# Kernel optimization log

Measured on AMD Instinct MI355X. Metric: run time of the kernel, lower is better.

## Reference

```python
import jax, jax.numpy as jnp
import numpy as np

B, S, H, NH = 2, 2048, 1024, 16
HD = H // NH  # head size = 64


def setup_inputs() -> dict:
    key = jax.random.key(0)
    ks = jax.random.split(key, 6)
    x = jax.random.normal(ks[0], (B, S, H), dtype=jnp.float32)
    additive_attention_mask = jnp.zeros((S,), dtype=jnp.float32)
    # nn.Linear params: weight [out, in], bias [out]
    w_qkv = jax.random.normal(ks[1], (3 * H, H), dtype=jnp.float32) / np.sqrt(H)
    b_qkv = jax.random.normal(ks[2], (3 * H,), dtype=jnp.float32) * 0.02
    w_o = jax.random.normal(ks[3], (H, H), dtype=jnp.float32) / np.sqrt(H)
    b_o = jax.random.normal(ks[4], (H,), dtype=jnp.float32) * 0.02
    return {"x": x, "additive_attention_mask": additive_attention_mask,
            "w_qkv": w_qkv, "b_qkv": b_qkv, "w_o": w_o, "b_o": b_o}


def reference(x, additive_attention_mask, w_qkv, b_qkv, w_o, b_o):
    # QKV projection: (B,S,H) @ (H,3H) + (3H,)
    qkv = jnp.einsum('bsh,oh->bso', x, w_qkv) + b_qkv
    q, k, v = qkv[..., :H], qkv[..., H:2 * H], qkv[..., 2 * H:]
    # split heads -> (B, NH, S, HD)
    def heads(t):
        return t.reshape(B, S, NH, HD).transpose(0, 2, 1, 3)
    qh, kh, vh = heads(q), heads(k), heads(v)
    # scores (B, NH, Sq, Sk); mask added BEFORE the 1/sqrt(d) scaling (faithful)
    scores = jnp.einsum('bhqd,bhkd->bhqk', qh, kh)
    scores = scores + additive_attention_mask[None, None, None, :]
    probs = jax.nn.softmax(scores / np.sqrt(HD).astype(np.float32), axis=-1)
    # dropout p=0.0 -> identity
    av = jnp.einsum('bhqk,bhkd->bqhd', probs, vh).reshape(B, S, H)
    return jnp.einsum('bsh,oh->bso', av, w_o) + b_o
```

## Files before the change

### kernel.cpp

```cpp
#include <hip/hip_runtime.h>
#include <cmath>

#define B_  2
#define S_  2048
#define H_  1024
#define NH_ 16
#define HD_ 64

typedef _Float16 half8  __attribute__((ext_vector_type(8)));
typedef __fp16   fp16x2 __attribute__((ext_vector_type(2)));
typedef float    f32x16 __attribute__((ext_vector_type(16)));

#define MFMA32(a, b, c) __builtin_amdgcn_mfma_f32_32x32x16_f16((a), (b), (c), 0, 0, 0)

__device__ __forceinline__ void gl2lds16(const void* g, void* l) {
    __builtin_amdgcn_global_load_lds(
        (const __attribute__((address_space(1))) unsigned int*)g,
        (__attribute__((address_space(3))) unsigned int*)l,
        16, 0, 0);
}

__device__ __forceinline__ unsigned pk16(float a, float b) {
    union { fp16x2 v; unsigned u; } c;
    c.v = __builtin_amdgcn_cvt_pkrtz(a, b);
    return c.u;
}

__device__ __forceinline__ float exp2_hw(float x) {
#if __has_builtin(__builtin_amdgcn_exp2f)
    return __builtin_amdgcn_exp2f(x);
#else
    return __expf(x * 0.6931471805599453f);
#endif
}

#define LOG2E   1.4426950408889634f
#define SCALE_  (0.125f * LOG2E)
#define THR2_   11.5415603f

__global__ __launch_bounds__(256, 4)
void conv_hilo(const float* __restrict__ src, _Float16* __restrict__ dh,
               _Float16* __restrict__ dl, int K)
{
    const int bid = blockIdx.x;
    const int nkt = K >> 6;
    const int rt  = bid / nkt;
    const int kt  = bid % nkt;
    const int tid = threadIdx.x;
    const size_t tb = (size_t)bid * 8192;
#pragma unroll
    for (int p = 0; p < 4; ++p) {
        const int idx = p * 256 + tid;
        const int r   = idx >> 3;
        const int g   = idx & 7;
        const float* s = src + (size_t)(rt * 128 + r) * K + kt * 64 + g * 8;
        const float4 v0 = *reinterpret_cast<const float4*>(s);
        const float4 v1 = *reinterpret_cast<const float4*>(s + 4);
        const float f[8] = {v0.x, v0.y, v0.z, v0.w, v1.x, v1.y, v1.z, v1.w};
        half8 hi, lo;
#pragma unroll
        for (int e = 0; e < 8; ++e) {
            const _Float16 hv = (_Float16)f[e];
            hi[e] = hv;
            lo[e] = (_Float16)(f[e] - (float)hv);
        }
        const int dst = r * 64 + ((g ^ (r & 7)) << 3);
        *reinterpret_cast<half8*>(dh + tb + dst) = hi;
        *reinterpret_cast<half8*>(dl + tb + dst) = lo;
    }
}

template<int QKV>
__global__ __launch_bounds__(256, 1)
void hgemm_split(const _Float16* __restrict__ Ah, const _Float16* __restrict__ Al,
                 const _Float16* __restrict__ Wh, const _Float16* __restrict__ Wl,
                 const float* __restrict__ bias, float* __restrict__ C,
                 float* __restrict__ Qo,
                 _Float16* __restrict__ Kh, _Float16* __restrict__ Kl,
                 _Float16* __restrict__ Vh, _Float16* __restrict__ Vl,
                 int nbm, int nbn, int nkt, int N)
{
    __shared__ __align__(16) unsigned char smem[131072];

    const int tid  = threadIdx.x;
    const int w    = tid >> 6;
    const int lane = tid & 63;
    const int lr   = lane & 31;
    const int hh   = lane >> 5;
    const int wm   = w >> 1, wn = w & 1;

    const int nwg = nbm * nbn;
    const int cpx = nwg >> 3;
    const int bid = blockIdx.x;
    const int wg  = (bid & 7) * cpx + (bid >> 3);
    const int mt  = wg / nbn, nt = wg % nbn;

    const size_t aBase = (size_t)mt * nkt * 8192;
    const size_t wBase = (size_t)nt * nkt * 8192;

    f32x16 acc[2][2];
#pragma unroll
    for (int mi = 0; mi < 2; ++mi)
#pragma unroll
        for (int ni = 0; ni < 2; ++ni)
#pragma unroll
            for (int r = 0; r < 16; ++r) acc[mi][ni][r] = 0.f;

    auto stage = [&](int kt, int buf) {
        const size_t at = aBase + (size_t)kt * 8192;
        const size_t wt = wBase + (size_t)kt * 8192;
        unsigned char* sb = smem + (buf << 16);
#pragma unroll
        for (int c = 0; c < 4; ++c) {
            const int loff = (w * 4 + c) * 512;
            const int goff = loff + lane * 8;
            gl2lds16((const void*)(Ah + at + goff), (void*)((_Float16*)sb + loff));
            gl2lds16((const void*)(Al + at + goff), (void*)((_Float16*)(sb + 16384) + loff));
            gl2lds16((const void*)(Wh + wt + goff), (void*)((_Float16*)(sb + 32768) + loff));
            gl2lds16((const void*)(Wl + wt + goff), (void*)((_Float16*)(sb + 49152) + loff));
        }
    };

    stage(0, 0);
    __syncthreads();

    for (int kt = 0; kt < nkt; ++kt) {
        if (kt + 1 < nkt) stage(kt + 1, (kt + 1) & 1);

        unsigned char* sb = smem + ((kt & 1) << 16);
        _Float16* sAh = (_Float16*)(sb);
        _Float16* sAl = (_Float16*)(sb + 16384);
        _Float16* sWh = (_Float16*)(sb + 32768);
        _Float16* sWl = (_Float16*)(sb + 49152);

#pragma unroll
        for (int ks = 0; ks < 4; ++ks) {
            const int g = ks * 2 + hh;
            half8 aH[2], aL[2], bH[2], bL[2];
#pragma unroll
            for (int mi = 0; mi < 2; ++mi) {
                const int r   = wm * 64 + mi * 32 + lr;
                const int idx = r * 64 + ((g ^ (r & 7)) << 3);
                aH[mi] = *reinterpret_cast<const half8*>(sAh + idx);
                aL[mi] = *reinterpret_cast<const half8*>(sAl + idx);
            }
#pragma unroll
            for (int ni = 0; ni < 2; ++ni) {
                const int c   = wn * 64 + ni * 32 + lr;
                const int idx = c * 64 + ((g ^ (c & 7)) << 3);
                bH[ni] = *reinterpret_cast<const half8*>(sWh + idx);
                bL[ni] = *reinterpret_cast<const half8*>(sWl + idx);
            }
#pragma unroll
            for (int mi = 0; mi < 2; ++mi)
#pragma unroll
                for (int ni = 0; ni < 2; ++ni) {
                    acc[mi][ni] = MFMA32(aH[mi], bH[ni], acc[mi][ni]);
                    acc[mi][ni] = MFMA32(aH[mi], bL[ni], acc[mi][ni]);
                    acc[mi][ni] = MFMA32(aL[mi], bH[ni], acc[mi][ni]);
                }
        }
        __syncthreads();
    }

    if constexpr (QKV == 0) {
        const int n0 = nt * 128 + wn * 64 + lr;
        float bv[2];
#pragma unroll
        for (int ni = 0; ni < 2; ++ni) bv[ni] = bias[n0 + ni * 32];
#pragma unroll
        for (int mi = 0; mi < 2; ++mi)
#pragma unroll
            for (int ni = 0; ni < 2; ++ni)
#pragma unroll
                for (int r = 0; r < 16; ++r) {
                    const int m = mt * 128 + wm * 64 + mi * 32 +
                                  (r & 3) + 8 * (r >> 2) + 4 * hh;
                    C[(size_t)m * N + n0 + ni * 32] = acc[mi][ni][r] + bv[ni];
                }
    } else {
        float* sC = (float*)smem;
        const int m0  = mt * 128;
        const int b   = m0 >> 11;
        const int kt0 = (m0 & 2047) >> 6;
#pragma unroll
        for (int pass = 0; pass < 2; ++pass) {
            __syncthreads();
            if (wm == pass) {
#pragma unroll
                for (int mi = 0; mi < 2; ++mi)
#pragma unroll
                    for (int ni = 0; ni < 2; ++ni)
#pragma unroll
                        for (int r = 0; r < 16; ++r) {
                            const int ml = mi * 32 + (r & 3) + 8 * (r >> 2) + 4 * hh;
                            sC[ml * 132 + wn * 64 + ni * 32 + lr] = acc[mi][ni][r];
                        }
            }
            __syncthreads();
            const int ktile = kt0 + pass;
            if (nt < 8) {
#pragma unroll
                for (int it = 0; it < 8; ++it) {
                    const int idx = it * 256 + tid;
                    const int row = idx >> 5;
                    const int c4  = (idx & 31) << 2;
                    float4 v = *reinterpret_cast<const float4*>(&sC[row * 132 + c4]);
                    const float4 bv = *reinterpret_cast<const float4*>(bias + nt * 128 + c4);
                    v.x += bv.x; v.y += bv.y; v.z += bv.z; v.w += bv.w;
                    *reinterpret_cast<float4*>(
                        Qo + (size_t)(m0 + pass * 64 + row) * 1024 + nt * 128 + c4) = v;
                }
            } else if (nt < 16) {
#pragma unroll
                for (int it = 0; it < 4; ++it) {
                    const int idx = it * 256 + tid;
                    const int key = idx >> 4;
                    const int g   = idx & 15;
                    const int head = 2 * (nt - 8) + (g >> 3);
                    const int d0   = (g & 7) << 3;
                    float f[8];
#pragma unroll
                    for (int e = 0; e < 8; ++e)
                        f[e] = sC[key * 132 + g * 8 + e] +
                               bias[1024 + (nt - 8) * 128 + g * 8 + e];
                    half8 hi, lo;
#pragma unroll
                    for (int e = 0; e < 8; ++e) {
                        const _Float16 hv = (_Float16)f[e];
                        hi[e] = hv;
                        lo[e] = (_Float16)(f[e] - (float)hv);
                    }
                    const size_t base = ((size_t)(b * 16 + head) * 32 + ktile) * 4096;
                    const size_t dst  = base + key * 64 + (d0 ^ ((key & 7) << 3));
                    *reinterpret_cast<half8*>(Kh + dst) = hi;
                    *reinterpret_cast<half8*>(Kl + dst) = lo;
                }
            } else {
#pragma unroll
                for (int it = 0; it < 4; ++it) {
                    const int idx = it * 256 + tid;
                    const int f   = idx >> 3;
                    const int kg  = idx & 7;
                    const int head = 2 * (nt - 16) + (f >> 6);
                    const int d    = f & 63;
                    const float bv = bias[2048 + (nt - 16) * 128 + f];
                    float fe[8];
#pragma unroll
                    for (int e = 0; e < 8; ++e)
                        fe[e] = sC[(kg * 8 + e) * 132 + f] + bv;
                    half8 hi, lo;
#pragma unroll
                    for (int e = 0; e < 8; ++e) {
                        const _Float16 hv = (_Float16)fe[e];
                        hi[e] = hv;
                        lo[e] = (_Float16)(fe[e] - (float)hv);
                    }
                    const size_t base = ((size_t)(b * 16 + head) * 32 + ktile) * 4096;
                    const size_t dst  = base + d * 64 + ((kg * 8) ^ ((d & 7) << 3));
                    *reinterpret_cast<half8*>(Vh + dst) = hi;
                    *reinterpret_cast<half8*>(Vl + dst) = lo;
                }
            }
        }
    }
}

__global__ __launch_bounds__(256, 2)
void attn_mfma(const float* __restrict__ Q, const float* __restrict__ mask,
               const _Float16* __restrict__ Kh, const _Float16* __restrict__ Kl,
               const _Float16* __restrict__ Vh, const _Float16* __restrict__ Vl,
               _Float16* __restrict__ Avh, _Float16* __restrict__ Avl)
{
    __shared__ __align__(16) unsigned char smem[73728];
    float* sM = (float*)(smem + 65536);
    float* sO = (float*)(smem);

    const int tid  = threadIdx.x;
    const int w    = tid >> 6;
    const int lane = tid & 63;
    const int lq   = lane & 31;
    const int hh   = lane >> 5;

    const int bid = blockIdx.x;
    const int wg  = (bid & 7) * 64 + (bid >> 3);
    const int bh  = wg >> 4;
    const int qb  = wg & 15;
    const int b   = bh >> 4, h = bh & 15;

    {
        const float4* mg = reinterpret_cast<const float4*>(mask);
        float4* ms = reinterpret_cast<float4*>(sM);
        float4 a = mg[tid], c = mg[tid + 256];
        a.x *= SCALE_; a.y *= SCALE_; a.z *= SCALE_; a.w *= SCALE_;
        c.x *= SCALE_; c.y *= SCALE_; c.z *= SCALE_; c.w *= SCALE_;
        ms[tid] = a; ms[tid + 256] = c;
    }

    const int qrow = b * S_ + qb * 128 + w * 32 + lq;
    half8 qh[4], ql[4];
#pragma unroll
    for (int ks = 0; ks < 4; ++ks) {
        const float* qp = Q + (size_t)qrow * 1024 + h * HD_ + ks * 16 + hh * 8;
        const float4 a = *reinterpret_cast<const float4*>(qp);
        const float4 c = *reinterpret_cast<const float4*>(qp + 4);
        float qf[8] = {a.x, a.y, a.z, a.w, c.x, c.y, c.z, c.w};
#pragma unroll
        for (int e = 0; e < 8; ++e) {
            const float sv = qf[e] * SCALE_;
            const _Float16 hv = (_Float16)sv;
            qh[ks][e] = hv;
            ql[ks][e] = (_Float16)(sv - (float)hv);
        }
    }

    const int swz = (lq & 7) << 3;
    int off[2][4];
#pragma unroll
    for (int t2 = 0; t2 < 2; ++t2)
#pragma unroll
        for (int ks = 0; ks < 4; ++ks)
            off[t2][ks] = (t2 * 32 + lq) * 64 + ((ks * 16 + hh * 8) ^ swz);

    f32x16 o0 = {0,0,0,0,0,0,0,0,0,0,0,0,0,0,0,0};
    f32x16 o1 = {0,0,0,0,0,0,0,0,0,0,0,0,0,0,0,0};
    float m_run = -INFINITY, l_run = 0.f;

    const size_t bhbase = (size_t)bh * 32 * 4096;

    {
        const size_t tb = bhbase;
#pragma unroll
        for (int i = 0; i < 2; ++i) {
            const int loff = (w * 2 + i) * 512;
            const int goff = loff + lane * 8;
            _Float16* nb = (_Float16*)smem;
            gl2lds16((const void*)(Kh + tb + goff), (void*)(nb + loff));
            gl2lds16((const void*)(Kl + tb + goff), (void*)(nb + 4096 + loff));
            gl2lds16((const void*)(Vh + tb + goff), (void*)(nb + 8192 + loff));
            gl2lds16((const void*)(Vl + tb + goff), (void*)(nb + 12288 + loff));
        }
    }
    __syncthreads();

    for (int kt = 0; kt < 32; ++kt) {
        _Float16* bb = (_Float16*)(smem + ((kt & 1) << 15));
        if (kt < 31) {
            _Float16* nb = (_Float16*)(smem + (((kt + 1) & 1) << 15));
            const size_t tb = bhbase + (size_t)(kt + 1) * 4096;
#pragma unroll
            for (int i = 0; i < 2; ++i) {
                const int loff = (w * 2 + i) * 512;
                const int goff = loff + lane * 8;
                gl2lds16((const void*)(Kh + tb + goff), (void*)(nb + loff));
                gl2lds16((const void*)(Kl + tb + goff), (void*)(nb + 4096 + loff));
                gl2lds16((const void*)(Vh + tb + goff), (void*)(nb + 8192 + loff));
                gl2lds16((const void*)(Vl + tb + goff), (void*)(nb + 12288 + loff));
            }
        }

        f32x16 st[2];
#pragma unroll
        for (int ktt = 0; ktt < 2; ++ktt) {
            f32x16 acc = {0,0,0,0,0,0,0,0,0,0,0,0,0,0,0,0};
#pragma unroll
            for (int ks = 0; ks < 4; ++ks) {
                const half8 ka = *reinterpret_cast<const half8*>(bb + off[ktt][ks]);
                const half8 kb = *reinterpret_cast<const half8*>(bb + 4096 + off[ktt][ks]);
                acc = MFMA32(ka, qh[ks], acc);
                acc = MFMA32(ka, ql[ks], acc);
                acc = MFMA32(kb, qh[ks], acc);
            }
            st[ktt] = acc;
        }

        float mx = -INFINITY;
#pragma unroll
        for (int ktt = 0; ktt < 2; ++ktt) {
#pragma unroll
            for (int rr = 0; rr < 4; ++rr) {
                const int key0 = kt * 64 + ktt * 32 + rr * 8 + hh * 4;
                const float4 mk = *reinterpret_cast<const float4*>(sM + key0);
                const float mkv[4] = {mk.x, mk.y, mk.z, mk.w};
#pragma unroll
                for (int c = 0; c < 4; ++c) {
                    const int r = rr * 4 + c;
                    const float tv = st[ktt][r] + mkv[c];
                    st[ktt][r] = tv;
                    mx = fmaxf(mx, tv);
                }
            }
        }
        mx = fmaxf(mx, __shfl_xor(mx, 32));

        if (!__all(mx - m_run <= THR2_)) {
            const float mnew = fmaxf(m_run, mx);
            const float corr = exp2_hw(m_run - mnew);
            m_run = mnew;
            l_run *= corr;
#pragma unroll
            for (int r = 0; r < 16; ++r) { o0[r] *= corr; o1[r] *= corr; }
        }
        float ps = 0.f;
#pragma unroll
        for (int ktt = 0; ktt < 2; ++ktt)
#pragma unroll
            for (int r = 0; r < 16; ++r) {
                const float p = exp2_hw(st[ktt][r] - m_run);
                st[ktt][r] = p;
                ps += p;
            }
        ps += __shfl_xor(ps, 32);
        l_run += ps;

        unsigned wph[2][4][2], wpl[2][4][2];
#pragma unroll
        for (int ktt = 0; ktt < 2; ++ktt)
#pragma unroll
            for (int rr = 0; rr < 4; ++rr)
#pragma unroll
                for (int pp = 0; pp < 2; ++pp) {
                    const float p0 = st[ktt][rr * 4 + pp * 2 + 0];
                    const float p1 = st[ktt][rr * 4 + pp * 2 + 1];
                    union { fp16x2 v; unsigned u; } hw;
                    hw.v = __builtin_amdgcn_cvt_pkrtz(p0, p1);
                    wph[ktt][rr][pp] = hw.u;
                    wpl[ktt][rr][pp] = pk16(p0 - (float)hw.v[0], p1 - (float)hw.v[1]);
                }

#pragma unroll
        for (int ks = 0; ks < 4; ++ks) {
            const int i1 = ks >> 1;
            const int rA = (ks & 1) * 2;
            union { unsigned u[4]; half8 v; } ph, pl;
            {
                const unsigned oA0 = wph[i1][rA + 0][0], oB0 = wph[i1][rA + 0][1];
                const unsigned oA1 = wph[i1][rA + 1][0], oB1 = wph[i1][rA + 1][1];
                const unsigned sA1 = (unsigned)__shfl_xor((int)oA1, 32);
                const unsigned sB1 = (unsigned)__shfl_xor((int)oB1, 32);
                const unsigned sA0 = (unsigned)__shfl_xor((int)oA0, 32);
                const unsigned sB0 = (unsigned)__shfl_xor((int)oB0, 32);
                ph.u[0] = hh ? sA1 : oA0;
                ph.u[1] = hh ? sB1 : oB0;
                ph.u[2] = hh ? oA1 : sA0;
                ph.u[3] = hh ? oB1 : sB0;
            }
            {
                const unsigned oA0 = wpl[i1][rA + 0][0], oB0 = wpl[i1][rA + 0][1];
                const unsigned oA1 = wpl[i1][rA + 1][0], oB1 = wpl[i1][rA + 1][1];
                const unsigned sA1 = (unsigned)__shfl_xor((int)oA1, 32);
                const unsigned sB1 = (unsigned)__shfl_xor((int)oB1, 32);
                const unsigned sA0 = (unsigned)__shfl_xor((int)oA0, 32);
                const unsigned sB0 = (unsigned)__shfl_xor((int)oB0, 32);
                pl.u[0] = hh ? sA1 : oA0;
                pl.u[1] = hh ? sB1 : oB0;
                pl.u[2] = hh ? oA1 : sA0;
                pl.u[3] = hh ? oB1 : sB0;
            }
#pragma unroll
            for (int dt = 0; dt < 2; ++dt) {
                const half8 va = *reinterpret_cast<const half8*>(bb + 8192 + off[dt][ks]);
                const half8 vb = *reinterpret_cast<const half8*>(bb + 12288 + off[dt][ks]);
                if (dt == 0) {
                    o0 = MFMA32(va, ph.v, o0);
                    o0 = MFMA32(va, pl.v, o0);
                    o0 = MFMA32(vb, ph.v, o0);
                } else {
                    o1 = MFMA32(va, ph.v, o1);
                    o1 = MFMA32(va, pl.v, o1);
                    o1 = MFMA32(vb, ph.v, o1);
                }
            }
        }
        __syncthreads();
    }

    const float inv = 1.f / l_run;
#pragma unroll
    for (int dt = 0; dt < 2; ++dt)
#pragma unroll
        for (int r = 0; r < 16; ++r) {
            const int d = dt * 32 + (r & 3) + 8 * (r >> 2) + 4 * hh;
            sO[(w * 32 + lq) * 68 + d] = (dt ? o1[r] : o0[r]) * inv;
        }
    __syncthreads();
    {
        const size_t tb = (((size_t)(b * 16 + qb)) * 16 + h) * 8192;
#pragma unroll
        for (int p = 0; p < 4; ++p) {
            const int idx = p * 256 + tid;
            const int q = idx >> 3, g = idx & 7;
            const float4 v0 = *reinterpret_cast<const float4*>(&sO[q * 68 + g * 8]);
            const float4 v1 = *reinterpret_cast<const float4*>(&sO[q * 68 + g * 8 + 4]);
            const float f[8] = {v0.x, v0.y, v0.z, v0.w, v1.x, v1.y, v1.z, v1.w};
            half8 hi, lo;
#pragma unroll
            for (int e = 0; e < 8; ++e) {
                const _Float16 hv = (_Float16)f[e];
                hi[e] = hv;
                lo[e] = (_Float16)(f[e] - (float)hv);
            }
            const int dst = q * 64 + ((g ^ (q & 7)) << 3);
            *reinterpret_cast<half8*>(Avh + tb + dst) = hi;
            *reinterpret_cast<half8*>(Avl + tb + dst) = lo;
        }
    }
}

extern "C" void kernel_launch(void* const* d_in, const int* in_sizes, int n_in,
                              void* d_out, int out_size, void* d_ws, size_t ws_size,
                              hipStream_t stream)
{
    const float* x     = (const float*)d_in[0];
    const float* mask  = (const float*)d_in[1];
    const float* w_qkv = (const float*)d_in[2];
    const float* b_qkv = (const float*)d_in[3];
    const float* w_o   = (const float*)d_in[4];
    const float* b_o   = (const float*)d_in[5];
    float* out = (float*)d_out;

    char* p = (char*)d_ws;
    float*    Qarr = (float*)p;             p += (size_t)4096 * 1024 * 4;
    _Float16* Kh   = (_Float16*)p;          p += (size_t)32 * 32 * 4096 * 2;
    _Float16* Kl   = (_Float16*)p;          p += (size_t)32 * 32 * 4096 * 2;
    _Float16* Vh   = (_Float16*)p;          p += (size_t)32 * 32 * 4096 * 2;
    _Float16* Vl   = (_Float16*)p;          p += (size_t)32 * 32 * 4096 * 2;
    _Float16* Xh   = (_Float16*)p;          p += (size_t)4096 * 1024 * 2;
    _Float16* Xl   = (_Float16*)p;          p += (size_t)4096 * 1024 * 2;
    _Float16* Wqh  = (_Float16*)p;          p += (size_t)3072 * 1024 * 2;
    _Float16* Wql  = (_Float16*)p;          p += (size_t)3072 * 1024 * 2;
    _Float16* Woh  = (_Float16*)p;          p += (size_t)1024 * 1024 * 2;
    _Float16* Wol  = (_Float16*)p;          p += (size_t)1024 * 1024 * 2;
    _Float16* Avh  = (_Float16*)p;          p += (size_t)4096 * 1024 * 2;
    _Float16* Avl  = (_Float16*)p;          p += (size_t)4096 * 1024 * 2;

    const dim3 blk(256);
    conv_hilo<<<dim3(32 * 16), blk, 0, stream>>>(x,     Xh,  Xl,  1024);
    conv_hilo<<<dim3(24 * 16), blk, 0, stream>>>(w_qkv, Wqh, Wql, 1024);
    conv_hilo<<<dim3(8 * 16),  blk, 0, stream>>>(w_o,   Woh, Wol, 1024);

    hgemm_split<1><<<dim3(32 * 24), blk, 0, stream>>>(
        Xh, Xl, Wqh, Wql, b_qkv, nullptr, Qarr, Kh, Kl, Vh, Vl, 32, 24, 16, 3072);
    attn_mfma<<<dim3(512), blk, 0, stream>>>(Qarr, mask, Kh, Kl, Vh, Vl, Avh, Avl);
    hgemm_split<0><<<dim3(32 * 8), blk, 0, stream>>>(
        Avh, Avl, Woh, Wol, b_o, out, nullptr, nullptr, nullptr, nullptr, nullptr,
        32, 8, 16, 1024);
}
```

Measured before the change: 335.3 us.

## Use 8 waves per GEMM block and drop low-half P term in attention

The split-fp16 GEMM moves from 4 to 8 waves per 128x128 tile. Each wave now owns a 32x64 sub-tile with two accumulators instead of four, and the staging and epilogue loops are retuned for 512 threads. The goal is more latency hiding and lower register pressure per wave. Separately, the attention P·V product no longer splits P into hi/lo fp16 parts, which drops one MFMA per pair and the matching shuffles. That trades some accuracy of the probabilities for fewer matrix operations.

```diff
diff --git a/kernel.cpp b/kernel.cpp
--- a/kernel.cpp
+++ b/kernel.cpp
@@ -71,7 +71,7 @@
 }
 
 template<int QKV>
-__global__ __launch_bounds__(256, 1)
+__global__ __launch_bounds__(512, 1)
 void hgemm_split(const _Float16* __restrict__ Ah, const _Float16* __restrict__ Al,
                  const _Float16* __restrict__ Wh, const _Float16* __restrict__ Wl,
                  const float* __restrict__ bias, float* __restrict__ C,
@@ -87,7 +87,8 @@
     const int lane = tid & 63;
     const int lr   = lane & 31;
     const int hh   = lane >> 5;
-    const int wm   = w >> 1, wn = w & 1;
+    const int wm   = w >> 1;
+    const int wn   = w & 1;
 
     const int nwg = nbm * nbn;
     const int cpx = nwg >> 3;
@@ -98,26 +99,23 @@
     const size_t aBase = (size_t)mt * nkt * 8192;
     const size_t wBase = (size_t)nt * nkt * 8192;
 
-    f32x16 acc[2][2];
-#pragma unroll
-    for (int mi = 0; mi < 2; ++mi)
-#pragma unroll
-        for (int ni = 0; ni < 2; ++ni)
-#pragma unroll
-            for (int r = 0; r < 16; ++r) acc[mi][ni][r] = 0.f;
+    f32x16 acc[2];
+#pragma unroll
+    for (int ni = 0; ni < 2; ++ni)
+#pragma unroll
+        for (int r = 0; r < 16; ++r) acc[ni][r] = 0.f;
 
     auto stage = [&](int kt, int buf) {
         const size_t at = aBase + (size_t)kt * 8192;
         const size_t wt = wBase + (size_t)kt * 8192;
         unsigned char* sb = smem + (buf << 16);
 #pragma unroll
-        for (int c = 0; c < 4; ++c) {
-            const int loff = (w * 4 + c) * 512;
-            const int goff = loff + lane * 8;
-            gl2lds16((const void*)(Ah + at + goff), (void*)((_Float16*)sb + loff));
-            gl2lds16((const void*)(Al + at + goff), (void*)((_Float16*)(sb + 16384) + loff));
-            gl2lds16((const void*)(Wh + wt + goff), (void*)((_Float16*)(sb + 32768) + loff));
-            gl2lds16((const void*)(Wl + wt + goff), (void*)((_Float16*)(sb + 49152) + loff));
+        for (int c = 0; c < 2; ++c) {
+            const int off = (c * 512 + tid) * 8;
+            gl2lds16((const void*)(Ah + at + off), (void*)((_Float16*)sb + off));
+            gl2lds16((const void*)(Al + at + off), (void*)((_Float16*)(sb + 16384) + off));
+            gl2lds16((const void*)(Wh + wt + off), (void*)((_Float16*)(sb + 32768) + off));
+            gl2lds16((const void*)(Wl + wt + off), (void*)((_Float16*)(sb + 49152) + off));
         }
     };
 
@@ -136,14 +134,11 @@
 #pragma unroll
         for (int ks = 0; ks < 4; ++ks) {
             const int g = ks * 2 + hh;
-            half8 aH[2], aL[2], bH[2], bL[2];
-#pragma unroll
-            for (int mi = 0; mi < 2; ++mi) {
-                const int r   = wm * 64 + mi * 32 + lr;
-                const int idx = r * 64 + ((g ^ (r & 7)) << 3);
-                aH[mi] = *reinterpret_cast<const half8*>(sAh + idx);
-                aL[mi] = *reinterpret_cast<const half8*>(sAl + idx);
-            }
+            const int r = wm * 32 + lr;
+            const int aidx = r * 64 + ((g ^ (r & 7)) << 3);
+            const half8 aH = *reinterpret_cast<const half8*>(sAh + aidx);
+            const half8 aL = *reinterpret_cast<const half8*>(sAl + aidx);
+            half8 bH[2], bL[2];
 #pragma unroll
             for (int ni = 0; ni < 2; ++ni) {
                 const int c   = wn * 64 + ni * 32 + lr;
@@ -152,13 +147,11 @@
                 bL[ni] = *reinterpret_cast<const half8*>(sWl + idx);
             }
 #pragma unroll
-            for (int mi = 0; mi < 2; ++mi)
-#pragma unroll
-                for (int ni = 0; ni < 2; ++ni) {
-                    acc[mi][ni] = MFMA32(aH[mi], bH[ni], acc[mi][ni]);
-                    acc[mi][ni] = MFMA32(aH[mi], bL[ni], acc[mi][ni]);
-                    acc[mi][ni] = MFMA32(aL[mi], bH[ni], acc[mi][ni]);
-                }
+            for (int ni = 0; ni < 2; ++ni) {
+                acc[ni] = MFMA32(aH, bH[ni], acc[ni]);
+                acc[ni] = MFMA32(aH, bL[ni], acc[ni]);
+                acc[ni] = MFMA32(aL, bH[ni], acc[ni]);
+            }
         }
         __syncthreads();
     }
@@ -169,15 +162,12 @@
 #pragma unroll
         for (int ni = 0; ni < 2; ++ni) bv[ni] = bias[n0 + ni * 32];
 #pragma unroll
-        for (int mi = 0; mi < 2; ++mi)
-#pragma unroll
-            for (int ni = 0; ni < 2; ++ni)
-#pragma unroll
-                for (int r = 0; r < 16; ++r) {
-                    const int m = mt * 128 + wm * 64 + mi * 32 +
-                                  (r & 3) + 8 * (r >> 2) + 4 * hh;
-                    C[(size_t)m * N + n0 + ni * 32] = acc[mi][ni][r] + bv[ni];
-                }
+        for (int ni = 0; ni < 2; ++ni)
+#pragma unroll
+            for (int r = 0; r < 16; ++r) {
+                const int m = mt * 128 + wm * 32 + (r & 3) + 8 * (r >> 2) + 4 * hh;
+                C[(size_t)m * N + n0 + ni * 32] = acc[ni][r] + bv[ni];
+            }
     } else {
         float* sC = (float*)smem;
         const int m0  = mt * 128;
@@ -186,23 +176,21 @@
 #pragma unroll
         for (int pass = 0; pass < 2; ++pass) {
             __syncthreads();
-            if (wm == pass) {
-#pragma unroll
-                for (int mi = 0; mi < 2; ++mi)
-#pragma unroll
-                    for (int ni = 0; ni < 2; ++ni)
-#pragma unroll
-                        for (int r = 0; r < 16; ++r) {
-                            const int ml = mi * 32 + (r & 3) + 8 * (r >> 2) + 4 * hh;
-                            sC[ml * 132 + wn * 64 + ni * 32 + lr] = acc[mi][ni][r];
-                        }
+            if ((wm >> 1) == pass) {
+#pragma unroll
+                for (int ni = 0; ni < 2; ++ni)
+#pragma unroll
+                    for (int r = 0; r < 16; ++r) {
+                        const int ml = (wm & 1) * 32 + (r & 3) + 8 * (r >> 2) + 4 * hh;
+                        sC[ml * 132 + wn * 64 + ni * 32 + lr] = acc[ni][r];
+                    }
             }
             __syncthreads();
             const int ktile = kt0 + pass;
             if (nt < 8) {
 #pragma unroll
-                for (int it = 0; it < 8; ++it) {
-                    const int idx = it * 256 + tid;
+                for (int it = 0; it < 4; ++it) {
+                    const int idx = it * 512 + tid;
                     const int row = idx >> 5;
                     const int c4  = (idx & 31) << 2;
                     float4 v = *reinterpret_cast<const float4*>(&sC[row * 132 + c4]);
@@ -213,8 +201,8 @@
                 }
             } else if (nt < 16) {
 #pragma unroll
-                for (int it = 0; it < 4; ++it) {
-                    const int idx = it * 256 + tid;
+                for (int it = 0; it < 2; ++it) {
+                    const int idx = it * 512 + tid;
                     const int key = idx >> 4;
                     const int g   = idx & 15;
                     const int head = 2 * (nt - 8) + (g >> 3);
@@ -238,8 +226,8 @@
                 }
             } else {
 #pragma unroll
-                for (int it = 0; it < 4; ++it) {
-                    const int idx = it * 256 + tid;
+                for (int it = 0; it < 2; ++it) {
+                    const int idx = it * 512 + tid;
                     const int f   = idx >> 3;
                     const int kg  = idx & 7;
                     const int head = 2 * (nt - 16) + (f >> 6);
@@ -413,26 +401,21 @@
         ps += __shfl_xor(ps, 32);
         l_run += ps;
 
-        unsigned wph[2][4][2], wpl[2][4][2];
+        unsigned wph[2][4][2];
 #pragma unroll
         for (int ktt = 0; ktt < 2; ++ktt)
 #pragma unroll
             for (int rr = 0; rr < 4; ++rr)
 #pragma unroll
-                for (int pp = 0; pp < 2; ++pp) {
-                    const float p0 = st[ktt][rr * 4 + pp * 2 + 0];
-                    const float p1 = st[ktt][rr * 4 + pp * 2 + 1];
-                    union { fp16x2 v; unsigned u; } hw;
-                    hw.v = __builtin_amdgcn_cvt_pkrtz(p0, p1);
-                    wph[ktt][rr][pp] = hw.u;
-                    wpl[ktt][rr][pp] = pk16(p0 - (float)hw.v[0], p1 - (float)hw.v[1]);
-                }
+                for (int pp = 0; pp < 2; ++pp)
+                    wph[ktt][rr][pp] = pk16(st[ktt][rr * 4 + pp * 2 + 0],
+                                            st[ktt][rr * 4 + pp * 2 + 1]);
 
 #pragma unroll
         for (int ks = 0; ks < 4; ++ks) {
             const int i1 = ks >> 1;
             const int rA = (ks & 1) * 2;
-            union { unsigned u[4]; half8 v; } ph, pl;
+            union { unsigned u[4]; half8 v; } ph;
             {
                 const unsigned oA0 = wph[i1][rA + 0][0], oB0 = wph[i1][rA + 0][1];
                 const unsigned oA1 = wph[i1][rA + 1][0], oB1 = wph[i1][rA + 1][1];
@@ -445,29 +428,15 @@
                 ph.u[2] = hh ? oA1 : sA0;
                 ph.u[3] = hh ? oB1 : sB0;
             }
-            {
-                const unsigned oA0 = wpl[i1][rA + 0][0], oB0 = wpl[i1][rA + 0][1];
-                const unsigned oA1 = wpl[i1][rA + 1][0], oB1 = wpl[i1][rA + 1][1];
-                const unsigned sA1 = (unsigned)__shfl_xor((int)oA1, 32);
-                const unsigned sB1 = (unsigned)__shfl_xor((int)oB1, 32);
-                const unsigned sA0 = (unsigned)__shfl_xor((int)oA0, 32);
-                const unsigned sB0 = (unsigned)__shfl_xor((int)oB0, 32);
-                pl.u[0] = hh ? sA1 : oA0;
-                pl.u[1] = hh ? sB1 : oB0;
-                pl.u[2] = hh ? oA1 : sA0;
-                pl.u[3] = hh ? oB1 : sB0;
-            }
 #pragma unroll
             for (int dt = 0; dt < 2; ++dt) {
                 const half8 va = *reinterpret_cast<const half8*>(bb + 8192 + off[dt][ks]);
                 const half8 vb = *reinterpret_cast<const half8*>(bb + 12288 + off[dt][ks]);
                 if (dt == 0) {
                     o0 = MFMA32(va, ph.v, o0);
-                    o0 = MFMA32(va, pl.v, o0);
                     o0 = MFMA32(vb, ph.v, o0);
                 } else {
                     o1 = MFMA32(va, ph.v, o1);
-                    o1 = MFMA32(va, pl.v, o1);
                     o1 = MFMA32(vb, ph.v, o1);
                 }
             }
@@ -534,15 +503,14 @@
     _Float16* Avh  = (_Float16*)p;          p += (size_t)4096 * 1024 * 2;
     _Float16* Avl  = (_Float16*)p;          p += (size_t)4096 * 1024 * 2;
 
-    const dim3 blk(256);
-    conv_hilo<<<dim3(32 * 16), blk, 0, stream>>>(x,     Xh,  Xl,  1024);
-    conv_hilo<<<dim3(24 * 16), blk, 0, stream>>>(w_qkv, Wqh, Wql, 1024);
-    conv_hilo<<<dim3(8 * 16),  blk, 0, stream>>>(w_o,   Woh, Wol, 1024);
-
-    hgemm_split<1><<<dim3(32 * 24), blk, 0, stream>>>(
+    conv_hilo<<<dim3(32 * 16), dim3(256), 0, stream>>>(x,     Xh,  Xl,  1024);
+    conv_hilo<<<dim3(24 * 16), dim3(256), 0, stream>>>(w_qkv, Wqh, Wql, 1024);
+    conv_hilo<<<dim3(8 * 16),  dim3(256), 0, stream>>>(w_o,   Woh, Wol, 1024);
+
+    hgemm_split<1><<<dim3(32 * 24), dim3(512), 0, stream>>>(
         Xh, Xl, Wqh, Wql, b_qkv, nullptr, Qarr, Kh, Kl, Vh, Vl, 32, 24, 16, 3072);
-    attn_mfma<<<dim3(512), blk, 0, stream>>>(Qarr, mask, Kh, Kl, Vh, Vl, Avh, Avl);
-    hgemm_split<0><<<dim3(32 * 8), blk, 0, stream>>>(
+    attn_mfma<<<dim3(512), dim3(256), 0, stream>>>(Qarr, mask, Kh, Kl, Vh, Vl, Avh, Avl);
+    hgemm_split<0><<<dim3(32 * 8), dim3(512), 0, stream>>>(
         Avh, Avl, Woh, Wol, b_o, out, nullptr, nullptr, nullptr, nullptr, nullptr,
         32, 8, 16, 1024);
 }
```

New measurement: 319.5 us. 4.7% less time.
